# Optimization experiments

Hardware: AMD Instinct MI355X
Metric: run time of the kernel (lower is better)

The kernel has to match this reference:

```python
import jax, jax.numpy as jnp
import numpy as np

TEMPERATURE = 0.5
EPS = 1e-12  # matches torch F.normalize clamp_min


def setup_inputs() -> dict:
    key = jax.random.key(0)
    k1, k2 = jax.random.split(key)
    N, D, C = 8192, 128, 64
    out_1 = jax.random.normal(k1, (N, D), dtype=jnp.float32)
    label = jax.random.randint(k2, (N,), 0, C, dtype=jnp.int64)
    return {"out_1": out_1, "label": label}


def reference(out_1, label):
    N = out_1.shape[0]
    # L2 normalize rows (F.normalize with eps clamp)
    norm = jnp.maximum(jnp.linalg.norm(out_1, axis=-1, keepdims=True), EPS)
    x = out_1 / norm
    # exp-scaled cosine similarity matrix [N, N]
    sim = jnp.exp(jnp.matmul(x, x.T) / TEMPERATURE)
    not_diag = 1.0 - jnp.eye(N, dtype=sim.dtype)
    # negatives: all off-diagonal entries per row
    negative_sim = jnp.sum(sim * not_diag, axis=-1)
    # positives: same label, excluding self; mean per row
    pos_mask = (label[:, None] == label[None, :]).astype(sim.dtype) * not_diag
    pos_count = jnp.sum(pos_mask, axis=-1)
    pos_sim = jnp.sum(sim * pos_mask, axis=-1) / pos_count
    return jnp.mean(-jnp.log(pos_sim / negative_sim))
```

## Files before the change

### kernel.cpp

```cpp
#include <hip/hip_runtime.h>
#include <hip/hip_bf16.h>
#include <stdint.h>

typedef __attribute__((ext_vector_type(8))) __bf16 bf16x8;
typedef __attribute__((ext_vector_type(16))) float floatx16;

#if __has_builtin(__builtin_amdgcn_exp2f)
#define EXP2F(x) __builtin_amdgcn_exp2f(x)
#else
#define EXP2F(x) exp2f(x)
#endif

#define GAS __attribute__((address_space(1)))
#define LAS __attribute__((address_space(3)))

#define SCALE_SQRT 1.69864359f
#define JCH 8

__global__ __launch_bounds__(256) void k_prep(const float* __restrict__ x,
                                              const int* __restrict__ raw,
                                              ushort* __restrict__ xb,
                                              int* __restrict__ lab, int N) {
  const int row = (blockIdx.x * 256 + threadIdx.x) >> 6;
  const int lane = threadIdx.x & 63;
  if (row >= N) return;
  const int probe = raw[2 * lane + 1];
  const bool is64 = (__ballot(probe != 0) == 0ull);
  const float2 v = ((const float2*)(x + (size_t)row * 128))[lane];
  float ss = v.x * v.x + v.y * v.y;
#pragma unroll
  for (int m = 1; m < 64; m <<= 1) ss += __shfl_xor(ss, m, 64);
  const float rn = SCALE_SQRT / fmaxf(sqrtf(ss), 1e-12f);
  __hip_bfloat162 o;
  o.x = __float2bfloat16(v.x * rn);
  o.y = __float2bfloat16(v.y * rn);
  ((__hip_bfloat162*)xb)[row * 64 + lane] = o;
  if (lane == 0) lab[row] = is64 ? raw[2 * row] : raw[row];
}

__global__ __launch_bounds__(256, 2) void k_sim(const ushort* __restrict__ xb,
                                                const int* __restrict__ lab,
                                                float* __restrict__ pneg,
                                                float* __restrict__ ppos,
                                                int N, int jpb) {
  __shared__ ushort ldsA[128 * 128];
  __shared__ ushort ldsB[2][64 * 128];
  const int tid = threadIdx.x;
  const int lane = tid & 63;
  const int wv = tid >> 6;
  const int wy = wv >> 1, wx = wv & 1;
  const int l31 = lane & 31, g2 = lane >> 5;
  const int l15 = lane & 15, g4 = lane >> 4;
  const int i0 = blockIdx.y * 128;
  const int c = blockIdx.x;
  const int jt0 = c * jpb;

  auto rowOff = [&](int t) -> int {
    const int reg = t & 15, mi = t >> 4;
    return wy * 64 + mi * 32 + (reg & 3) + 8 * (reg >> 2) + 4 * g2;
  };

#pragma unroll
  for (int it = 0; it < 8; ++it) {
    const int r0 = it * 16 + wv * 4;
    const int lr = r0 + g4;
    const int kb = l15 ^ (lr & 15);
    const ushort* gp = xb + (size_t)(i0 + lr) * 128 + kb * 8;
    __builtin_amdgcn_global_load_lds((GAS void*)gp, (LAS void*)&ldsA[r0 * 128], 16, 0, 0);
  }
  {
    const int j0 = jt0 * 64;
#pragma unroll
    for (int it = 0; it < 4; ++it) {
      const int r0 = it * 16 + wv * 4;
      const int lr = r0 + g4;
      const int kb = l15 ^ (lr & 15);
      const ushort* gp = xb + (size_t)(j0 + lr) * 128 + kb * 8;
      __builtin_amdgcn_global_load_lds((GAS void*)gp, (LAS void*)&ldsB[0][r0 * 128], 16, 0, 0);
    }
  }

  int li[32];
  float neg[32], pos[32];
#pragma unroll
  for (int t = 0; t < 32; ++t) {
    li[t] = lab[i0 + rowOff(t)];
    neg[t] = 0.0f;
    pos[t] = 0.0f;
  }
  __syncthreads();

  for (int t = 0; t < jpb; ++t) {
    const int j0 = (jt0 + t) * 64;
    const int buf = t & 1;
    if (t + 1 < jpb) {
      const int jn = j0 + 64;
#pragma unroll
      for (int it = 0; it < 4; ++it) {
        const int r0 = it * 16 + wv * 4;
        const int lr = r0 + g4;
        const int kb = l15 ^ (lr & 15);
        const ushort* gp = xb + (size_t)(jn + lr) * 128 + kb * 8;
        __builtin_amdgcn_global_load_lds((GAS void*)gp, (LAS void*)&ldsB[buf ^ 1][r0 * 128], 16, 0, 0);
      }
    }
    const int lj = lab[j0 + wx * 32 + l31];

    floatx16 acc[2];
    acc[0] = (floatx16)(0.0f);
    acc[1] = (floatx16)(0.0f);
#pragma unroll
    for (int kt = 0; kt < 8; ++kt) {
      const int brow = wx * 32 + l31;
      const int bkb = (kt * 2 + g2) ^ (brow & 15);
      const bf16x8 bfr = *(const bf16x8*)&ldsB[buf][brow * 128 + bkb * 8];
#pragma unroll
      for (int mi = 0; mi < 2; ++mi) {
        const int arow = wy * 64 + mi * 32 + l31;
        const int akb = (kt * 2 + g2) ^ (arow & 15);
        const bf16x8 af = *(const bf16x8*)&ldsA[arow * 128 + akb * 8];
        acc[mi] = __builtin_amdgcn_mfma_f32_32x32x16_bf16(af, bfr, acc[mi], 0, 0, 0);
      }
    }

    const int dlt = j0 - i0;
    const bool diag = ((unsigned)dlt < 128u);
    const int jc = wx * 32 + l31 + dlt;
    auto epi = [&](bool DG) {
#pragma unroll
      for (int mi = 0; mi < 2; ++mi) {
#pragma unroll
        for (int reg = 0; reg < 16; ++reg) {
          float e = EXP2F(acc[mi][reg]);
          if (DG) {
            const int ir = wy * 64 + mi * 32 + (reg & 3) + 8 * (reg >> 2) + 4 * g2;
            if (ir == jc) e = 0.0f;
          }
          neg[mi * 16 + reg] += e;
          pos[mi * 16 + reg] += (li[mi * 16 + reg] == lj) ? e : 0.0f;
        }
      }
    };
    if (diag) epi(true); else epi(false);
    __syncthreads();
  }

  float* fl = (float*)ldsB;
#pragma unroll
  for (int t = 0; t < 32; ++t) {
    float n = neg[t], p = pos[t];
#pragma unroll
    for (int m = 1; m < 32; m <<= 1) {
      n += __shfl_xor(n, m, 64);
      p += __shfl_xor(p, m, 64);
    }
    if (l31 == 0) {
      const int r = rowOff(t);
      fl[(r * 2 + 0) * 2 + wx] = n;
      fl[(r * 2 + 1) * 2 + wx] = p;
    }
  }
  __syncthreads();
  if (tid < 128) {
    const int r = tid;
    pneg[(size_t)c * N + i0 + r] = fl[(r * 2 + 0) * 2] + fl[(r * 2 + 0) * 2 + 1];
    ppos[(size_t)c * N + i0 + r] = fl[(r * 2 + 1) * 2] + fl[(r * 2 + 1) * 2 + 1];
  }
}

__global__ __launch_bounds__(1024) void k_final(const float* __restrict__ pneg,
                                                const float* __restrict__ ppos,
                                                const int* __restrict__ lab,
                                                float* __restrict__ out, int N) {
  __shared__ int h[64];
  if (threadIdx.x < 64) h[threadIdx.x] = 0;
  __syncthreads();
  for (int i = threadIdx.x; i < N; i += 1024) atomicAdd(&h[lab[i] & 63], 1);
  __syncthreads();
  double s = 0.0;
  for (int i = threadIdx.x; i < N; i += 1024) {
    float n = 0.0f, p = 0.0f;
#pragma unroll
    for (int c = 0; c < JCH; ++c) {
      n += pneg[(size_t)c * N + i];
      p += ppos[(size_t)c * N + i];
    }
    const float cnt = (float)(h[lab[i] & 63] - 1);
    s += (double)logf(n * cnt / p);
  }
#pragma unroll
  for (int m = 1; m < 64; m <<= 1) s += __shfl_xor(s, m, 64);
  __shared__ double wsum[16];
  if ((threadIdx.x & 63) == 0) wsum[threadIdx.x >> 6] = s;
  __syncthreads();
  if (threadIdx.x == 0) {
    double tot = 0.0;
    for (int w = 0; w < 16; ++w) tot += wsum[w];
    out[0] = (float)(tot / (double)N);
  }
}

extern "C" void kernel_launch(void* const* d_in, const int* in_sizes, int n_in,
                              void* d_out, int out_size, void* d_ws, size_t ws_size,
                              hipStream_t stream) {
  const float* x = (const float*)d_in[0];
  const int* raw_label = (const int*)d_in[1];
  const int N = in_sizes[1];
  char* ws = (char*)d_ws;
  ushort* xb = (ushort*)ws;
  float* pneg = (float*)(ws + (size_t)N * 128 * 2);
  float* ppos = pneg + (size_t)JCH * N;
  int* lab = (int*)(ppos + (size_t)JCH * N);
  float* out = (float*)d_out;

  const int jpb = (N / 64) / JCH;

  k_prep<<<dim3(N / 4), dim3(256), 0, stream>>>(x, raw_label, xb, lab, N);
  k_sim<<<dim3(JCH, N / 128), dim3(256), 0, stream>>>(xb, lab, pneg, ppos, N, jpb);
  k_final<<<dim3(1), dim3(1024), 0, stream>>>(pneg, ppos, lab, out, N);
}
```

Measured before the change: 101.7 us.

## Sort rows by label so most tiles skip positive-mask epilogue

Adds a counting sort of rows by label (per-block histogram, scan, scatter) so the normalized bf16 rows are stored grouped by class. In the similarity kernel, column tiles that cannot share a label with the row block take a cheap exp-and-sum path with no label compare or diagonal check. A-operand fragments are now held in registers across the j loop, the loop count is a compile-time constant, and labels are packed into bytes. Class counts for the final reduction come from the scan output instead of a histogram. The cost is two extra small kernel launches, a serial single-block scan, and higher register pressure that may lower occupancy.

```diff
diff --git a/kernel.cpp b/kernel.cpp
--- a/kernel.cpp
+++ b/kernel.cpp
@@ -16,16 +16,61 @@
 
 #define SCALE_SQRT 1.69864359f
 #define JCH 8
+#define JPB 16
+
+__global__ __launch_bounds__(256) void k_sort1(const int* __restrict__ raw,
+                                               int* __restrict__ lab,
+                                               int* __restrict__ ranks,
+                                               int* __restrict__ cnt, int N) {
+  __shared__ int h[64];
+  __shared__ int s64;
+  const int r = blockIdx.x * 256 + threadIdx.x;
+  if (threadIdx.x < 64) {
+    h[threadIdx.x] = 0;
+    const int probe = raw[2 * threadIdx.x + 1];
+    const unsigned long long b = __ballot(probe != 0);
+    if (threadIdx.x == 0) s64 = (b == 0ull);
+  }
+  __syncthreads();
+  const int l = (s64 ? raw[2 * r] : raw[r]) & 63;
+  lab[r] = l;
+  ranks[r] = atomicAdd(&h[l], 1);
+  __syncthreads();
+  if (threadIdx.x < 64) cnt[blockIdx.x * 64 + threadIdx.x] = h[threadIdx.x];
+}
+
+__global__ __launch_bounds__(256) void k_scan(const int* __restrict__ cnt,
+                                              int* __restrict__ base,
+                                              int* __restrict__ cum, int N) {
+  __shared__ int tot[64];
+  const int k = threadIdx.x;
+  const int nch = N >> 8;
+  if (k < 64) {
+    int run = 0;
+    for (int c = 0; c < nch; ++c) { base[c * 64 + k] = run; run += cnt[c * 64 + k]; }
+    tot[k] = run;
+  }
+  __syncthreads();
+  if (k == 0) {
+    int run = 0;
+    for (int i = 0; i < 64; ++i) { cum[i] = run; run += tot[i]; }
+    cum[64] = run;
+  }
+  __syncthreads();
+  for (int i = threadIdx.x; i < nch * 64; i += 256) base[i] += cum[i & 63];
+}
 
 __global__ __launch_bounds__(256) void k_prep(const float* __restrict__ x,
-                                              const int* __restrict__ raw,
+                                              const int* __restrict__ lab,
+                                              const int* __restrict__ ranks,
+                                              const int* __restrict__ base,
                                               ushort* __restrict__ xb,
-                                              int* __restrict__ lab, int N) {
+                                              int* __restrict__ labs, int N) {
   const int row = (blockIdx.x * 256 + threadIdx.x) >> 6;
   const int lane = threadIdx.x & 63;
   if (row >= N) return;
-  const int probe = raw[2 * lane + 1];
-  const bool is64 = (__ballot(probe != 0) == 0ull);
+  const int l = lab[row];
+  const int slot = base[(row >> 8) * 64 + l] + ranks[row];
   const float2 v = ((const float2*)(x + (size_t)row * 128))[lane];
   float ss = v.x * v.x + v.y * v.y;
 #pragma unroll
@@ -34,15 +79,15 @@
   __hip_bfloat162 o;
   o.x = __float2bfloat16(v.x * rn);
   o.y = __float2bfloat16(v.y * rn);
-  ((__hip_bfloat162*)xb)[row * 64 + lane] = o;
-  if (lane == 0) lab[row] = is64 ? raw[2 * row] : raw[row];
+  ((__hip_bfloat162*)xb)[slot * 64 + lane] = o;
+  if (lane == 0) labs[slot] = l;
 }
 
 __global__ __launch_bounds__(256, 2) void k_sim(const ushort* __restrict__ xb,
-                                                const int* __restrict__ lab,
+                                                const int* __restrict__ labs,
+                                                const int* __restrict__ cum,
                                                 float* __restrict__ pneg,
-                                                float* __restrict__ ppos,
-                                                int N, int jpb) {
+                                                float* __restrict__ ppos, int N) {
   __shared__ ushort ldsA[128 * 128];
   __shared__ ushort ldsB[2][64 * 128];
   const int tid = threadIdx.x;
@@ -53,7 +98,7 @@
   const int l15 = lane & 15, g4 = lane >> 4;
   const int i0 = blockIdx.y * 128;
   const int c = blockIdx.x;
-  const int jt0 = c * jpb;
+  const int jt0 = c * JPB;
 
   auto rowOff = [&](int t) -> int {
     const int reg = t & 15, mi = t >> 4;
@@ -80,20 +125,45 @@
     }
   }
 
-  int li[32];
+  const int ps = cum[labs[i0]];
+  const int pe = cum[labs[i0 + 127] + 1];
+
+  int li_pack[8];
+#pragma unroll
+  for (int q = 0; q < 8; ++q) li_pack[q] = 0;
+#pragma unroll
+  for (int t = 0; t < 32; ++t)
+    li_pack[t >> 2] |= labs[i0 + rowOff(t)] << ((t & 3) * 8);
+
   float neg[32], pos[32];
 #pragma unroll
-  for (int t = 0; t < 32; ++t) {
-    li[t] = lab[i0 + rowOff(t)];
-    neg[t] = 0.0f;
-    pos[t] = 0.0f;
-  }
-  __syncthreads();
-
-  for (int t = 0; t < jpb; ++t) {
+  for (int t = 0; t < 32; ++t) { neg[t] = 0.0f; pos[t] = 0.0f; }
+
+  __syncthreads();
+
+  bf16x8 afr[2][8];
+#pragma unroll
+  for (int mi = 0; mi < 2; ++mi) {
+    const int arow = wy * 64 + mi * 32 + l31;
+#pragma unroll
+    for (int kt = 0; kt < 8; ++kt) {
+      const int akb = (kt * 2 + g2) ^ (arow & 15);
+      afr[mi][kt] = *(const bf16x8*)&ldsA[arow * 128 + akb * 8];
+    }
+  }
+  int baddr[8];
+  {
+    const int brow = wx * 32 + l31;
+#pragma unroll
+    for (int kt = 0; kt < 8; ++kt)
+      baddr[kt] = brow * 128 + (((kt * 2 + g2) ^ (brow & 15)) * 8);
+  }
+
+#pragma unroll
+  for (int t = 0; t < JPB; ++t) {
     const int j0 = (jt0 + t) * 64;
     const int buf = t & 1;
-    if (t + 1 < jpb) {
+    if (t + 1 < JPB) {
       const int jn = j0 + 64;
 #pragma unroll
       for (int it = 0; it < 4; ++it) {
@@ -104,44 +174,48 @@
         __builtin_amdgcn_global_load_lds((GAS void*)gp, (LAS void*)&ldsB[buf ^ 1][r0 * 128], 16, 0, 0);
       }
     }
-    const int lj = lab[j0 + wx * 32 + l31];
 
     floatx16 acc[2];
     acc[0] = (floatx16)(0.0f);
     acc[1] = (floatx16)(0.0f);
 #pragma unroll
     for (int kt = 0; kt < 8; ++kt) {
-      const int brow = wx * 32 + l31;
-      const int bkb = (kt * 2 + g2) ^ (brow & 15);
-      const bf16x8 bfr = *(const bf16x8*)&ldsB[buf][brow * 128 + bkb * 8];
-#pragma unroll
-      for (int mi = 0; mi < 2; ++mi) {
-        const int arow = wy * 64 + mi * 32 + l31;
-        const int akb = (kt * 2 + g2) ^ (arow & 15);
-        const bf16x8 af = *(const bf16x8*)&ldsA[arow * 128 + akb * 8];
-        acc[mi] = __builtin_amdgcn_mfma_f32_32x32x16_bf16(af, bfr, acc[mi], 0, 0, 0);
-      }
-    }
-
-    const int dlt = j0 - i0;
-    const bool diag = ((unsigned)dlt < 128u);
-    const int jc = wx * 32 + l31 + dlt;
-    auto epi = [&](bool DG) {
-#pragma unroll
-      for (int mi = 0; mi < 2; ++mi) {
-#pragma unroll
-        for (int reg = 0; reg < 16; ++reg) {
-          float e = EXP2F(acc[mi][reg]);
-          if (DG) {
-            const int ir = wy * 64 + mi * 32 + (reg & 3) + 8 * (reg >> 2) + 4 * g2;
-            if (ir == jc) e = 0.0f;
+      const bf16x8 bfr = *(const bf16x8*)&ldsB[buf][baddr[kt]];
+      acc[0] = __builtin_amdgcn_mfma_f32_32x32x16_bf16(afr[0][kt], bfr, acc[0], 0, 0, 0);
+      acc[1] = __builtin_amdgcn_mfma_f32_32x32x16_bf16(afr[1][kt], bfr, acc[1], 0, 0, 0);
+    }
+
+    const bool posT = (j0 < pe) && (j0 + 64 > ps);
+    if (!posT) {
+#pragma unroll
+      for (int mi = 0; mi < 2; ++mi)
+#pragma unroll
+        for (int reg = 0; reg < 16; ++reg)
+          neg[mi * 16 + reg] += EXP2F(acc[mi][reg]);
+    } else {
+      const int lj = labs[j0 + wx * 32 + l31];
+      const int dlt = j0 - i0;
+      const bool dg = ((unsigned)dlt < 128u);
+      const int jc = wx * 32 + l31 + dlt;
+      auto epi = [&](bool DG) {
+#pragma unroll
+        for (int mi = 0; mi < 2; ++mi) {
+#pragma unroll
+          for (int reg = 0; reg < 16; ++reg) {
+            const int t2 = mi * 16 + reg;
+            float e = EXP2F(acc[mi][reg]);
+            if (DG) {
+              const int ir = wy * 64 + mi * 32 + (reg & 3) + 8 * (reg >> 2) + 4 * g2;
+              if (ir == jc) e = 0.0f;
+            }
+            const int liq = (li_pack[t2 >> 2] >> ((t2 & 3) * 8)) & 63;
+            neg[t2] += e;
+            pos[t2] += (liq == lj) ? e : 0.0f;
           }
-          neg[mi * 16 + reg] += e;
-          pos[mi * 16 + reg] += (li[mi * 16 + reg] == lj) ? e : 0.0f;
         }
-      }
-    };
-    if (diag) epi(true); else epi(false);
+      };
+      if (dg) epi(true); else epi(false);
+    }
     __syncthreads();
   }
 
@@ -170,13 +244,9 @@
 
 __global__ __launch_bounds__(1024) void k_final(const float* __restrict__ pneg,
                                                 const float* __restrict__ ppos,
-                                                const int* __restrict__ lab,
+                                                const int* __restrict__ labs,
+                                                const int* __restrict__ cum,
                                                 float* __restrict__ out, int N) {
-  __shared__ int h[64];
-  if (threadIdx.x < 64) h[threadIdx.x] = 0;
-  __syncthreads();
-  for (int i = threadIdx.x; i < N; i += 1024) atomicAdd(&h[lab[i] & 63], 1);
-  __syncthreads();
   double s = 0.0;
   for (int i = threadIdx.x; i < N; i += 1024) {
     float n = 0.0f, p = 0.0f;
@@ -185,7 +255,8 @@
       n += pneg[(size_t)c * N + i];
       p += ppos[(size_t)c * N + i];
     }
-    const float cnt = (float)(h[lab[i] & 63] - 1);
+    const int l = labs[i];
+    const float cnt = (float)(cum[l + 1] - cum[l] - 1);
     s += (double)logf(n * cnt / p);
   }
 #pragma unroll
@@ -211,11 +282,16 @@
   float* pneg = (float*)(ws + (size_t)N * 128 * 2);
   float* ppos = pneg + (size_t)JCH * N;
   int* lab = (int*)(ppos + (size_t)JCH * N);
+  int* ranks = lab + N;
+  int* labs = ranks + N;
+  int* cnt = labs + N;
+  int* base = cnt + (N >> 8) * 64;
+  int* cum = base + (N >> 8) * 64;
   float* out = (float*)d_out;
 
-  const int jpb = (N / 64) / JCH;
-
-  k_prep<<<dim3(N / 4), dim3(256), 0, stream>>>(x, raw_label, xb, lab, N);
-  k_sim<<<dim3(JCH, N / 128), dim3(256), 0, stream>>>(xb, lab, pneg, ppos, N, jpb);
-  k_final<<<dim3(1), dim3(1024), 0, stream>>>(pneg, ppos, lab, out, N);
-}
+  k_sort1<<<dim3(N / 256), dim3(256), 0, stream>>>(raw_label, lab, ranks, cnt, N);
+  k_scan<<<dim3(1), dim3(256), 0, stream>>>(cnt, base, cum, N);
+  k_prep<<<dim3(N / 4), dim3(256), 0, stream>>>(x, lab, ranks, base, xb, labs, N);
+  k_sim<<<dim3(JCH, N / 128), dim3(256), 0, stream>>>(xb, labs, cum, pneg, ppos, N);
+  k_final<<<dim3(1), dim3(1024), 0, stream>>>(pneg, ppos, labs, cum, out, N);
+}
```

Result: slower. 131.3 us (+29.2%).
